# Optimization experiments

Hardware: AMD Instinct MI355X
Metric: run time of the kernel (lower is better)

Reference implementation:

```python
import jax, jax.numpy as jnp
import numpy as np

D = 192

def layer_norm(x, g, b, eps=1e-5):
    m = jnp.mean(x, -1, keepdims=True)
    v = jnp.var(x, -1, keepdims=True)
    return (x - m) * jax.lax.rsqrt(v + eps) * g + b

def _bilinear(v, x, y, H, W):
    # v: (N, nH, H*W, hd); x, y: (N, nH, Q) fractional pixel coords (grid_sample, align_corners=False, zero pad)
    x0 = jnp.floor(x); y0 = jnp.floor(y)
    wx = x - x0; wy = y - y0
    x0i = x0.astype(jnp.int32); y0i = y0.astype(jnp.int32)
    def gather(xi, yi):
        valid = (xi >= 0) & (xi < W) & (yi >= 0) & (yi < H)
        idx = jnp.clip(yi, 0, H - 1) * W + jnp.clip(xi, 0, W - 1)
        g = jnp.take_along_axis(v, idx[..., None], axis=2)
        return jnp.where(valid[..., None], g, 0.0)
    return (gather(x0i, y0i) * ((1 - wx) * (1 - wy))[..., None]
            + gather(x0i + 1, y0i) * (wx * (1 - wy))[..., None]
            + gather(x0i, y0i + 1) * ((1 - wx) * wy)[..., None]
            + gather(x0i + 1, y0i + 1) * (wx * wy)[..., None])

def _linear1d(v, p, T):
    # v: (N, nH, T, hd); p: (N, nH, Q) fractional temporal coords
    p0 = jnp.floor(p); wp = p - p0; p0i = p0.astype(jnp.int32)
    def gather(pi):
        valid = (pi >= 0) & (pi < T)
        idx = jnp.clip(pi, 0, T - 1)
        g = jnp.take_along_axis(v, idx[..., None], axis=2)
        return jnp.where(valid[..., None], g, 0.0)
    return gather(p0i) * (1 - wp)[..., None] + gather(p0i + 1) * wp[..., None]

def msdeform_2d(q, ref, H, W, nH, P, off_w, off_b, aw_w, aw_b, v_w, v_b, o_w, o_b):
    # single-level MSDeformAttn; q == input_flatten (self-attn style usage)
    N, L, d = q.shape; hd = d // nH
    v = (q @ v_w + v_b).reshape(N, L, nH, hd).transpose(0, 2, 1, 3)  # (N,nH,L,hd)
    off = (q @ off_w + off_b).reshape(N, L, nH, P, 2)
    aw = jax.nn.softmax((q @ aw_w + aw_b).reshape(N, L, nH, P), axis=-1)
    norm = jnp.array([W, H], dtype=q.dtype)
    loc = ref[:, :, None, :, :] + off / norm  # (N,L,nH,P,2)
    x = (loc[..., 0] * W - 0.5).transpose(0, 2, 1, 3).reshape(N, nH, L * P)
    y = (loc[..., 1] * H - 0.5).transpose(0, 2, 1, 3).reshape(N, nH, L * P)
    samp = _bilinear(v, x, y, H, W).reshape(N, nH, L, P, hd)
    out = jnp.einsum('nlhp,nhlpd->nlhd', aw, samp).reshape(N, L, d)
    return out @ o_w + o_b

def msdeform_1d(q, ref, T, nH, P, off_w, off_b, aw_w, aw_b, v_w, v_b, o_w, o_b):
    N, L, d = q.shape; hd = d // nH  # L == T
    v = (q @ v_w + v_b).reshape(N, L, nH, hd).transpose(0, 2, 1, 3)
    off = (q @ off_w + off_b).reshape(N, L, nH, P)
    aw = jax.nn.softmax((q @ aw_w + aw_b).reshape(N, L, nH, P), axis=-1)
    loc = ref[:, :, 0, 0][:, :, None, None] + off / T  # (N,L,nH,P)
    p = (loc * T - 0.5).transpose(0, 2, 1, 3).reshape(N, nH, L * P)
    samp = _linear1d(v, p, T).reshape(N, nH, L, P, hd)
    out = jnp.einsum('nlhp,nhlpd->nlhd', aw, samp).reshape(N, L, d)
    return out @ o_w + o_b

def setup_inputs():
    key = jax.random.key(0)
    ks = jax.random.split(key, 24)
    d = D; n, t, h, w = 2, 8, 48, 48
    f = lambda k, shape, s=0.05: jax.random.normal(k, shape, dtype=jnp.float32) * s
    return {
        'x': jax.random.normal(ks[0], (n, d, t, h, w), dtype=jnp.float32),
        'fuse': jax.random.normal(ks[1], (n, d, h, w), dtype=jnp.float32),
        'conv_w': f(ks[2], (d, 2 * d)), 'conv_b': f(ks[3], (d,)),
        's_off_w': f(ks[4], (d, 16 * 2 * 2), 0.01), 's_off_b': f(ks[5], (16 * 2 * 2,), 0.01),
        's_aw_w': f(ks[6], (d, 16 * 2)), 's_aw_b': f(ks[7], (16 * 2,)),
        's_v_w': f(ks[8], (d, d)), 's_v_b': f(ks[9], (d,)),
        's_o_w': f(ks[10], (d, d)), 's_o_b': f(ks[11], (d,)),
        't_off_w': f(ks[12], (d, 8 * 4), 0.01), 't_off_b': f(ks[13], (8 * 4,), 0.01),
        't_aw_w': f(ks[14], (d, 8 * 4)), 't_aw_b': f(ks[15], (8 * 4,)),
        't_v_w': f(ks[16], (d, d)), 't_v_b': f(ks[17], (d,)),
        't_o_w': f(ks[18], (d, d)), 't_o_b': f(ks[19], (d,)),
        'ln1_g': jnp.ones((d,), jnp.float32), 'ln1_b': jnp.zeros((d,), jnp.float32),
        'ln2_g': jnp.ones((d,), jnp.float32), 'ln2_b': jnp.zeros((d,), jnp.float32),
        'ln3_g': jnp.ones((d,), jnp.float32), 'ln3_b': jnp.zeros((d,), jnp.float32),
        'lin1_w': f(ks[20], (2 * d, d)), 'lin1_b': f(ks[21], (d,)),
        'lin2_w': f(ks[22], (d, d)), 'lin2_b': f(ks[23], (d,)),
    }

def reference(x, fuse, conv_w, conv_b, s_off_w, s_off_b, s_aw_w, s_aw_b, s_v_w, s_v_b, s_o_w, s_o_b,
              t_off_w, t_off_b, t_aw_w, t_aw_b, t_v_w, t_v_b, t_o_w, t_o_b,
              ln1_g, ln1_b, ln2_g, ln2_b, ln3_g, ln3_b, lin1_w, lin1_b, lin2_w, lin2_b):
    n, c, t, h, w = x.shape; d = c
    fuse_e = jnp.broadcast_to(fuse[:, :, None, :, :], (n, c, t, h, w))
    xc = jnp.concatenate([x, fuse_e], axis=1)                      # (n,2c,t,h,w)
    xm = jnp.einsum('ncthw,oc->nothw', xc, conv_w) + conv_b[None, :, None, None, None]
    # spatial deformable attention over h*w tokens per (n*t)
    x_space = xm.transpose(0, 2, 3, 4, 1).reshape(n * t, h * w, d)
    yy, xx = jnp.meshgrid(jnp.linspace(0, 1, h, dtype=x.dtype), jnp.linspace(0, 1, w, dtype=x.dtype), indexing='ij')
    ref2 = jnp.broadcast_to(jnp.stack([yy, xx], -1).reshape(1, h * w, 1, 2), (n * t, h * w, 1, 2))
    s_out = msdeform_2d(x_space, ref2, h, w, 16, 2, s_off_w, s_off_b, s_aw_w, s_aw_b, s_v_w, s_v_b, s_o_w, s_o_b)
    # temporal deformable attention over t tokens per (n*h*w)
    x_temp = xm.transpose(0, 3, 4, 1, 2).reshape(n * h * w, t, d)
    ref1 = jnp.broadcast_to(jnp.linspace(0, 1, t, dtype=x.dtype).reshape(1, t, 1, 1), (n * h * w, t, 1, 1))
    t_out = msdeform_1d(x_temp, ref1, t, 8, 4, t_off_w, t_off_b, t_aw_w, t_aw_b, t_v_w, t_v_b, t_o_w, t_o_b)
    # residual + LN, then the original's raw .view(h*w, t, n, c) reinterpretation (replicated faithfully)
    xs = layer_norm(x_space + s_out, ln1_g, ln1_b)
    xs = xs.reshape(h * w, t, n, d).transpose(1, 0, 2, 3).reshape(t * h * w, n, d)
    xt = layer_norm(x_temp + t_out, ln2_g, ln2_b)
    xt = xt.reshape(h * w, t, n, d).transpose(1, 0, 2, 3).reshape(t * h * w, n, d)
    x_st = jnp.concatenate([xt, xs], axis=-1)                      # (t*h*w, n, 2d)
    x_st = jax.nn.gelu(x_st @ lin1_w + lin1_b, approximate=False) @ lin2_w + lin2_b
    x_st = x_st.reshape(t, h, w, n, d).transpose(3, 4, 0, 1, 2)    # (n,d,t,h,w)
    xm = xm + x_st
    out = layer_norm(xm.transpose(0, 2, 3, 4, 1), ln3_g, ln3_b).transpose(0, 4, 1, 2, 3)
    return out
```

## Files before the change

### kernel.cpp

```cpp
#include <hip/hip_runtime.h>
#include <hip/hip_bf16.h>
#include <math.h>

typedef __hip_bfloat16 bf16;
typedef __attribute__((ext_vector_type(8))) short bf16x8;
typedef __attribute__((ext_vector_type(4))) float f32x4;

#define N_    2
#define D_    192
#define T_    8
#define H_    48
#define W_    48
#define HW_   2304
#define NPOS  36864
#define BUF_ELEMS 7077888

#define OFF_SOFFW 0
#define OFF_SOFFB 12288
#define OFF_SAWW  12352
#define OFF_SAWB  18496
#define OFF_SVW   18528
#define OFF_SVB   55392
#define OFF_SOW   55584
#define OFF_SOB   92448
#define OFF_TOFFW 92640
#define OFF_TOFFB 98784
#define OFF_TAWW  98816
#define OFF_TAWB  104960
#define OFF_TVW   104992
#define OFF_TVB   141856
#define OFF_TOW   142048
#define OFF_TOB   178912
#define OFF_LN1G  179104
#define OFF_LN1B  179296
#define OFF_LN2G  179488
#define OFF_LN2B  179680
#define OFF_LN3G  179872
#define OFF_LN3B  180064
#define OFF_LIN1W 180256
#define OFF_LIN1B 253984
#define OFF_LIN2W 254176
#define OFF_LIN2B 291040
#define OFF_CONVB 291232
#define WF_TOTAL  291424

#define PB_SCOMB 0
#define PB_SOW   55296
#define PB_TCOMB 92160
#define PB_TOW   141312
#define PB_LIN1  178176
#define PB_CONV  251904
#define PB_LIN2  325632
#define PB_TOTAL 362496

static __device__ __forceinline__ float b2f(bf16 v){ return __bfloat162float(v); }
static __device__ __forceinline__ bf16  f2b(float v){ return __float2bfloat16(v); }
static __device__ __forceinline__ float lo16(unsigned u){
  unsigned v = u<<16; return *(float*)&v;
}
static __device__ __forceinline__ float hi16(unsigned u){
  unsigned v = u & 0xFFFF0000u; return *(float*)&v;
}
static __device__ __forceinline__ unsigned pk2(float a, float b){
  bf16 x = f2b(a), y = f2b(b);
  return (unsigned)*(unsigned short*)&x | ((unsigned)*(unsigned short*)&y << 16);
}
static __device__ __forceinline__ int detect_bf(const void* ln1g){
  unsigned u = *(const unsigned*)ln1g;
  return __builtin_amdgcn_readfirstlane(((u & 0xFFFFu) != 0u) ? 1 : 0);
}
static __device__ __forceinline__ int swz8(int ch, int r){ return ch ^ (r & 7); }

struct KPtrs { const void* p[27]; };
static __device__ const int WSZ[27] = {12288,64,6144,32,36864,192,36864,192,
  6144,32,6144,32,36864,192,36864,192, 192,192,192,192,192,192, 73728,192,36864,192, 192};

__global__ void k_cvtw(KPtrs P, float* __restrict__ WF, const void* __restrict__ ln1g){
  int bf = detect_bf(ln1g);
  int gid = blockIdx.x*256 + threadIdx.x;
  if (gid >= WF_TOTAL) return;
  int e = 0, off = 0;
  while (gid >= off + WSZ[e]){ off += WSZ[e]; ++e; }
  int i = gid - off;
  WF[gid] = bf ? b2f(((const bf16*)P.p[e])[i]) : ((const float*)P.p[e])[i];
}

__global__ void k_wt(const void* __restrict__ W, float* __restrict__ Wt, const void* __restrict__ ln1g){
  int bf = detect_bf(ln1g);
  int i = blockIdx.x*256 + threadIdx.x;
  if (i < 384*192){
    int c = i/192, o = i%192;
    Wt[i] = bf ? b2f(((const bf16*)W)[o*384+c]) : ((const float*)W)[o*384+c];
  }
}

__global__ void k_packB(const float* __restrict__ WF, const float* __restrict__ Wt,
                        bf16* __restrict__ PB){
  const int NB[7]  = {108,72,96,72,144,144,72};
  const int NT[7]  = {18,12,16,12,12,12,12};
  const int DST[7] = {PB_SCOMB, PB_SOW, PB_TCOMB, PB_TOW, PB_LIN1, PB_CONV, PB_LIN2};
  int bid = blockIdx.x, e = 0, start = 0;
  while (e < 6 && bid >= start + NB[e]){ start += NB[e]; ++e; }
  int local = bid - start;
  int nt = local % NT[e], kt = local / NT[e];
  int l = threadIdx.x;
  int k0 = kt*32 + (l>>4)*8, n0 = nt*16 + (l&15);
  bf16* D = PB + DST[e] + ((long)(kt*NT[e]+nt)*64 + l)*8;
  #pragma unroll
  for (int i=0;i<8;++i){
    int k = k0 + i;
    float v;
    if (e==0){
      if (n0<192)      v = WF[OFF_SVW  + k*192 + n0];
      else if (n0<256) v = WF[OFF_SOFFW+ k*64  + (n0-192)];
      else             v = WF[OFF_SAWW + k*32  + (n0-256)];
    } else if (e==1)   v = WF[OFF_SOW  + k*192 + n0];
    else if (e==2){
      if (n0<192)      v = WF[OFF_TVW  + k*192 + n0];
      else if (n0<224) v = WF[OFF_TOFFW+ k*32  + (n0-192)];
      else             v = WF[OFF_TAWW + k*32  + (n0-224)];
    } else if (e==3)   v = WF[OFF_TOW  + k*192 + n0];
    else if (e==4)     v = WF[OFF_LIN1W+ k*192 + n0];
    else if (e==5)     v = Wt[k*192 + n0];
    else               v = WF[OFF_LIN2W+ k*192 + n0];
    D[i] = f2b(v);
  }
}

template<int KTOT, int MODE, int CF32>
__global__ void __launch_bounds__(256) k_gemm(const bf16* __restrict__ A0, const bf16* __restrict__ A1,
      const bf16* __restrict__ Bp, const float* __restrict__ bias, void* __restrict__ C_){
  __shared__ bf16 sA[64*KTOT];
  const int NCH = KTOT/8;
  int tid = threadIdx.x;
  int r0 = blockIdx.x*64;
  for (int i=tid; i<64*NCH; i+=256){
    int r = i/NCH, ch = i - r*NCH;
    int grow;
    if (MODE==1){
      int q = r0+r, f = q>>1, n2 = q&1;
      int t2 = f/HW_, hw2 = f - t2*HW_;
      grow = hw2*16 + t2*2 + n2;
    } else grow = r0+r;
    const bf16* src = (MODE==1 && ch>=24) ? (A1 + (long)grow*192 + (ch-24)*8)
                                          : (A0 + (long)grow*192 + ch*8);
    *(bf16x8*)(sA + r*KTOT + swz8(ch,r)*8) = *(const bf16x8*)src;
  }
  __syncthreads();
  int wid = tid>>6, lane = tid&63;
  int m16 = lane&15, kg = lane>>4;
  f32x4 acc[4][3];
  #pragma unroll
  for (int mi=0;mi<4;++mi)
    #pragma unroll
    for (int ni=0;ni<3;++ni) acc[mi][ni] = (f32x4){0.f,0.f,0.f,0.f};

  const int NKT = KTOT/32;
  for (int kt=0; kt<NKT; ++kt){
    bf16x8 b[3];
    #pragma unroll
    for (int ni=0;ni<3;++ni){
      int nt = wid*3 + ni;
      b[ni] = *(const bf16x8*)(Bp + ((long)(kt*12+nt)*64 + lane)*8);
    }
    bf16x8 a[4];
    #pragma unroll
    for (int mi=0;mi<4;++mi){
      int row = mi*16 + m16;
      a[mi] = *(const bf16x8*)(sA + row*KTOT + swz8(kt*4+kg,row)*8);
    }
    #pragma unroll
    for (int mi=0;mi<4;++mi)
      #pragma unroll
      for (int ni=0;ni<3;++ni)
        acc[mi][ni] = __builtin_amdgcn_mfma_f32_16x16x32_bf16(a[mi], b[ni], acc[mi][ni], 0,0,0);
  }
  const float IS2 = 0.70710678118654752f;
  #pragma unroll
  for (int mi=0;mi<4;++mi)
    #pragma unroll
    for (int ni=0;ni<3;++ni){
      int col = (wid*3+ni)*16 + m16;
      float bv = bias[col];
      #pragma unroll
      for (int rg=0;rg<4;++rg){
        int row = r0 + mi*16 + kg*4 + rg;
        float v = acc[mi][ni][rg] + bv;
        if (MODE==1) v = 0.5f*v*(1.f+erff(v*IS2));
        if (CF32) ((float*)C_)[(long)row*192 + col] = v;
        else      ((bf16*)C_)[(long)row*192 + col] = f2b(v);
      }
    }
}

template<int NWAVES, int NTW, int NO>
__global__ void __launch_bounds__(NWAVES*64) k_gemmC(const float* __restrict__ A,
      const bf16* __restrict__ Bp, const float* __restrict__ biasV,
      const float* __restrict__ biasO, const float* __restrict__ biasA,
      bf16* __restrict__ Cv, float* __restrict__ Coa){
  __shared__ bf16 sA[64*192];
  const int NT_TOT = NWAVES*NTW;
  const int NOA = NT_TOT*16 - 192;
  int tid = threadIdx.x;
  int r0 = blockIdx.x*64;
  for (int i=tid; i<64*48; i+=NWAVES*64){
    int r = i/48, c4 = i - r*48;
    float4 v = *(const float4*)(A + (long)(r0+r)*192 + c4*4);
    bf16* dst = sA + r*192 + swz8(c4>>1, r)*8 + (c4&1)*4;
    dst[0]=f2b(v.x); dst[1]=f2b(v.y); dst[2]=f2b(v.z); dst[3]=f2b(v.w);
  }
  __syncthreads();
  int wid = tid>>6, lane = tid&63;
  int m16 = lane&15, kg = lane>>4;
  f32x4 acc[4][NTW];
  #pragma unroll
  for (int mi=0;mi<4;++mi)
    #pragma unroll
    for (int ni=0;ni<NTW;++ni) acc[mi][ni] = (f32x4){0.f,0.f,0.f,0.f};
  for (int kt=0; kt<6; ++kt){
    bf16x8 b[NTW];
    #pragma unroll
    for (int ni=0;ni<NTW;++ni){
      int nt = wid*NTW + ni;
      b[ni] = *(const bf16x8*)(Bp + ((long)(kt*NT_TOT+nt)*64 + lane)*8);
    }
    bf16x8 a[4];
    #pragma unroll
    for (int mi=0;mi<4;++mi){
      int row = mi*16 + m16;
      a[mi] = *(const bf16x8*)(sA + row*192 + swz8(kt*4+kg,row)*8);
    }
    #pragma unroll
    for (int mi=0;mi<4;++mi)
      #pragma unroll
      for (int ni=0;ni<NTW;++ni)
        acc[mi][ni] = __builtin_amdgcn_mfma_f32_16x16x32_bf16(a[mi], b[ni], acc[mi][ni], 0,0,0);
  }
  #pragma unroll
  for (int mi=0;mi<4;++mi)
    #pragma unroll
    for (int ni=0;ni<NTW;++ni){
      int col = (wid*NTW+ni)*16 + m16;
      #pragma unroll
      for (int rg=0;rg<4;++rg){
        int row = r0 + mi*16 + kg*4 + rg;
        float v = acc[mi][ni][rg];
        if (col < 192)           Cv[(long)row*192 + col] = f2b(v + biasV[col]);
        else if (col < 192+NO)   Coa[(long)row*NOA + (col-192)] = v + biasO[col-192];
        else                     Coa[(long)row*NOA + (col-192)] = v + biasA[col-192-NO];
      }
    }
}

__global__ void __launch_bounds__(256) k_convm(const void* __restrict__ x, const void* __restrict__ fuse,
      const bf16* __restrict__ Bp, const float* __restrict__ bias, float* __restrict__ B0,
      const void* __restrict__ ln1g){
  __shared__ bf16 sA[64*384];
  int bf = detect_bf(ln1g);
  int bid = blockIdx.x;
  int n = bid/(8*36), rm = bid%(8*36);
  int t = rm/36, hb = rm%36;
  int hw0 = hb*64;
  int tid = threadIdx.x;
  if (bf){
    for (int i=tid; i<384*64; i+=256){
      int c = i>>6, j = i&63;
      long idx = (c<192) ? ((long)((n*192+c)*8 + t)*HW_ + hw0 + j)
                         : ((long)(n*192+(c-192))*HW_ + hw0 + j);
      bf16 v = ((const bf16*)((c<192)?x:fuse))[idx];
      sA[j*384 + swz8(c>>3, j)*8 + (c&7)] = v;
    }
  } else {
    for (int i=tid; i<384*64; i+=256){
      int c = i>>6, j = i&63;
      long idx = (c<192) ? ((long)((n*192+c)*8 + t)*HW_ + hw0 + j)
                         : ((long)(n*192+(c-192))*HW_ + hw0 + j);
      float v = ((const float*)((c<192)?x:fuse))[idx];
      sA[j*384 + swz8(c>>3, j)*8 + (c&7)] = f2b(v);
    }
  }
  __syncthreads();
  int wid = tid>>6, lane = tid&63;
  int m16 = lane&15, kg = lane>>4;
  f32x4 acc[4][3];
  #pragma unroll
  for (int mi=0;mi<4;++mi)
    #pragma unroll
    for (int ni=0;ni<3;++ni) acc[mi][ni] = (f32x4){0.f,0.f,0.f,0.f};
  for (int kt=0; kt<12; ++kt){
    bf16x8 b[3];
    #pragma unroll
    for (int ni=0;ni<3;++ni){
      int nt = wid*3 + ni;
      b[ni] = *(const bf16x8*)(Bp + ((long)(kt*12+nt)*64 + lane)*8);
    }
    bf16x8 a[4];
    #pragma unroll
    for (int mi=0;mi<4;++mi){
      int row = mi*16 + m16;
      a[mi] = *(const bf16x8*)(&sA[row*384 + swz8(kt*4+kg,row)*8]);
    }
    #pragma unroll
    for (int mi=0;mi<4;++mi)
      #pragma unroll
      for (int ni=0;ni<3;++ni)
        acc[mi][ni] = __builtin_amdgcn_mfma_f32_16x16x32_bf16(a[mi], b[ni], acc[mi][ni], 0,0,0);
  }
  long posbase = (long)(n*8+t)*HW_ + hw0;
  #pragma unroll
  for (int mi=0;mi<4;++mi)
    #pragma unroll
    for (int ni=0;ni<3;++ni){
      int col = (wid*3+ni)*16 + m16;
      float bv = bias[col];
      #pragma unroll
      for (int rg=0;rg<4;++rg){
        int row = mi*16 + kg*4 + rg;
        B0[(posbase + row)*192 + col] = acc[mi][ni][rg] + bv;
      }
    }
}

__global__ void __launch_bounds__(256) k_xt(const float* __restrict__ S0, float* __restrict__ S4){
  __shared__ float s[8*1536];
  int b0 = blockIdx.x*8, tid = threadIdx.x;
  for (int i=tid; i<8*1536; i+=256){
    int j = i/1536, rest = i - j*1536;
    int t = rest/192, o = rest - t*192;
    int b = b0 + j;
    int n = b/HW_, hw = b - n*HW_;
    s[j*1536 + (o/24)*192 + (o%24)*8 + t] = S0[((long)((n*8+t)*HW_) + hw)*192 + o];
  }
  __syncthreads();
  for (int i=tid; i<8*1536; i+=256){
    int j = i/1536, rest = i - j*1536;
    S4[(long)(b0+j)*1536 + rest] = s[j*1536 + rest];
  }
}

__global__ void __launch_bounds__(256) k_samp_s(const float* __restrict__ OA, const bf16* __restrict__ V,
    bf16* __restrict__ out){
  __shared__ float tup[512][8];
  int r0 = blockIdx.x*16, tid = threadIdx.x;
  int nt = r0 / HW_;
  {
    int row = tid>>4, head = tid&15;
    int l = (r0+row) % HW_;
    int iy = l/48, jx = l%48;
    const float* oa = OA + (long)(r0+row)*96;
    float l0 = oa[64+head*2], l1 = oa[64+head*2+1];
    float m = fmaxf(l0,l1);
    float e0 = __expf(l0-m), e1 = __expf(l1-m);
    float inv = 1.f/(e0+e1);
    const float SC = 48.0f/47.0f;
    #pragma unroll
    for (int p=0;p<2;++p){
      float aw = (p==0?e0:e1)*inv;
      float fx = iy*SC + oa[head*4+p*2+0] - 0.5f;
      float fy = jx*SC + oa[head*4+p*2+1] - 0.5f;
      float x0f = floorf(fx), y0f = floorf(fy);
      float wx = fx-x0f, wy = fy-y0f;
      int x0 = (int)x0f, y0 = (int)y0f;
      int x1 = x0+1, y1 = y0+1;
      bool vx0 = (x0>=0 && x0<48), vx1 = (x1>=0 && x1<48);
      bool vy0 = (y0>=0 && y0<48), vy1 = (y1>=0 && y1<48);
      int cx0 = min(max(x0,0),47), cx1 = min(max(x1,0),47);
      int cy0 = min(max(y0,0),47), cy1 = min(max(y1,0),47);
      float* tp = tup[row*32 + head*2 + p];
      tp[0] = (vx0&&vy0) ? aw*(1.f-wx)*(1.f-wy) : 0.f;
      tp[1] = (vx1&&vy0) ? aw*wx*(1.f-wy)       : 0.f;
      tp[2] = (vx0&&vy1) ? aw*(1.f-wx)*wy       : 0.f;
      tp[3] = (vx1&&vy1) ? aw*wx*wy             : 0.f;
      tp[4] = (float)(cy0*48+cx0);
      tp[5] = (float)(cy0*48+cx1);
      tp[6] = (float)(cy1*48+cx0);
      tp[7] = (float)(cy1*48+cx1);
    }
  }
  __syncthreads();
  const unsigned* vbu = (const unsigned*)(V + (long)nt*HW_*192);
  for (int it=tid; it<1536; it+=256){
    int row = it/96, cp = it - row*96;
    int head = cp/6;
    float a0 = 0.f, a1 = 0.f;
    #pragma unroll
    for (int p=0;p<2;++p){
      const float* tp = tup[row*32 + head*2 + p];
      #pragma unroll
      for (int c=0;c<4;++c){
        float w = tp[c];
        int idx = (int)tp[4+c];
        unsigned u = vbu[idx*96 + cp];
        a0 += w*lo16(u);
        a1 += w*hi16(u);
      }
    }
    ((unsigned*)out)[(long)(r0+row)*96 + cp] = pk2(a0, a1);
  }
}

__global__ void __launch_bounds__(256) k_samp_t(const float* __restrict__ OT, const bf16* __restrict__ V,
    bf16* __restrict__ out){
  __shared__ float tup[512][4];
  __shared__ unsigned sV[1536];
  int r0 = blockIdx.x*16, tid = threadIdx.x;
  int b0 = r0 >> 3;
  if (tid < 128){
    int row = tid>>3, head = tid&7;
    int tau = (r0+row) & 7;
    float pref = tau*(8.0f/7.0f) - 0.5f;
    const float* ot = OT + (long)(r0+row)*64;
    float l0=ot[32+head*4], l1=ot[32+head*4+1], l2=ot[32+head*4+2], l3=ot[32+head*4+3];
    float m = fmaxf(fmaxf(l0,l1), fmaxf(l2,l3));
    float e0=__expf(l0-m), e1=__expf(l1-m), e2=__expf(l2-m), e3=__expf(l3-m);
    float inv = 1.f/(e0+e1+e2+e3);
    float ee[4] = {e0,e1,e2,e3};
    #pragma unroll
    for (int p=0;p<4;++p){
      float aw = ee[p]*inv;
      float fp = pref + ot[head*4+p];
      float p0f = floorf(fp);
      float wp = fp - p0f;
      int p0 = (int)p0f, p1 = p0+1;
      float* tp = tup[row*32 + head*4 + p];
      tp[0] = (p0>=0 && p0<8) ? aw*(1.f-wp) : 0.f;
      tp[1] = (p1>=0 && p1<8) ? aw*wp       : 0.f;
      tp[2] = (float)min(max(p0,0),7);
      tp[3] = (float)min(max(p1,0),7);
    }
  } else {
    const unsigned* Vu = (const unsigned*)(V + (long)b0*1536);
    for (int i=tid-128; i<1536; i+=128) sV[i] = Vu[i];
  }
  __syncthreads();
  for (int it=tid; it<1536; it+=256){
    int row = it/96, cp = it - row*96;
    int head = cp/12;
    const unsigned* vb = sV + (row>>3)*768;
    float a0 = 0.f, a1 = 0.f;
    #pragma unroll
    for (int p=0;p<4;++p){
      const float* tp = tup[row*32 + head*4 + p];
      unsigned u0 = vb[(int)tp[2]*96 + cp];
      unsigned u1 = vb[(int)tp[3]*96 + cp];
      a0 += tp[0]*lo16(u0) + tp[1]*lo16(u1);
      a1 += tp[0]*hi16(u0) + tp[1]*hi16(u1);
    }
    ((unsigned*)out)[(long)(r0+row)*96 + cp] = pk2(a0, a1);
  }
}

__global__ void __launch_bounds__(256) k_addln(const float* __restrict__ X, const bf16* __restrict__ Y,
    const float* __restrict__ g, const float* __restrict__ bta, bf16* __restrict__ out){
  int r = blockIdx.x*4 + (threadIdx.x>>6);
  int lane = threadIdx.x & 63;
  float v[3]; float s=0.f, s2=0.f;
  #pragma unroll
  for (int e=0;e<3;++e){
    int c = lane*3+e;
    float y = X[(long)r*192+c] + b2f(Y[(long)r*192+c]);
    v[e]=y; s+=y; s2+=y*y;
  }
  #pragma unroll
  for (int off=32; off>0; off>>=1){ s += __shfl_xor(s,off); s2 += __shfl_xor(s2,off); }
  float mean = s*(1.f/192.f);
  float rstd = rsqrtf(s2*(1.f/192.f) - mean*mean + 1e-5f);
  #pragma unroll
  for (int e=0;e<3;++e){
    int c = lane*3+e;
    out[(long)r*192+c] = f2b((v[e]-mean)*rstd*g[c] + bta[c]);
  }
}

__global__ void __launch_bounds__(256) k_final3(const float* __restrict__ B0, const bf16* __restrict__ hid,
    const bf16* __restrict__ Bp, const float* __restrict__ bias2,
    const float* __restrict__ g, const float* __restrict__ bta,
    void* __restrict__ out, const void* __restrict__ ln1g){
  __shared__ float yb[32][193];
  __shared__ float mrs[32][2];
  bf16* sA = (bf16*)&yb[0][0];
  int bf = detect_bf(ln1g);
  int pos0 = blockIdx.x*32;
  int tid = threadIdx.x, wid = tid>>6, lane = tid&63;
  int m16 = lane&15, kg = lane>>4;
  int n2 = pos0/(T_*HW_), rem0 = pos0%(T_*HW_);
  long qrow0 = (long)rem0*2 + n2;
  for (int i=tid; i<32*24; i+=256){
    int r = i/24, ch = i - r*24;
    *(bf16x8*)(sA + r*192 + swz8(ch,r)*8) =
        *(const bf16x8*)(hid + (qrow0 + r*2)*192 + ch*8);
  }
  __syncthreads();
  f32x4 acc[2][3];
  #pragma unroll
  for (int mi=0;mi<2;++mi)
    #pragma unroll
    for (int ni=0;ni<3;++ni) acc[mi][ni] = (f32x4){0.f,0.f,0.f,0.f};
  for (int kt=0; kt<6; ++kt){
    bf16x8 b[3];
    #pragma unroll
    for (int ni=0;ni<3;++ni){
      int nt = wid*3 + ni;
      b[ni] = *(const bf16x8*)(Bp + ((long)(kt*12+nt)*64 + lane)*8);
    }
    bf16x8 a[2];
    #pragma unroll
    for (int mi=0;mi<2;++mi){
      int row = mi*16 + m16;
      a[mi] = *(const bf16x8*)(sA + row*192 + swz8(kt*4+kg,row)*8);
    }
    #pragma unroll
    for (int mi=0;mi<2;++mi)
      #pragma unroll
      for (int ni=0;ni<3;++ni)
        acc[mi][ni] = __builtin_amdgcn_mfma_f32_16x16x32_bf16(a[mi], b[ni], acc[mi][ni], 0,0,0);
  }
  __syncthreads();
  #pragma unroll
  for (int mi=0;mi<2;++mi)
    #pragma unroll
    for (int ni=0;ni<3;++ni){
      int col = (wid*3+ni)*16 + m16;
      float bv = bias2[col];
      #pragma unroll
      for (int rg=0;rg<4;++rg){
        int lr = mi*16 + kg*4 + rg;
        yb[lr][col] = acc[mi][ni][rg] + bv + B0[(long)(pos0+lr)*192 + col];
      }
    }
  __syncthreads();
  for (int rr=0; rr<8; ++rr){
    int row = wid*8 + rr;
    float s=0.f, s2=0.f;
    #pragma unroll
    for (int e=0;e<3;++e){
      float v = yb[row][lane*3+e];
      s += v; s2 += v*v;
    }
    #pragma unroll
    for (int off=32; off>0; off>>=1){ s += __shfl_xor(s,off); s2 += __shfl_xor(s2,off); }
    if (lane==0){
      float mean = s*(1.f/192.f);
      mrs[row][0] = mean;
      mrs[row][1] = rsqrtf(s2*(1.f/192.f) - mean*mean + 1e-5f);
    }
  }
  __syncthreads();
  int t2 = rem0/HW_, hw0 = rem0%HW_;
  int j = lane & 31;
  float mean = mrs[j][0], rstd = mrs[j][1];
  for (int cc=0; cc<48; cc+=2){
    int c = wid*48 + cc + (lane>>5);
    float val = (yb[j][c]-mean)*rstd*g[c] + bta[c];
    long idx = ((long)(n2*192 + c)*8 + t2)*HW_ + hw0 + j;
    if (bf) ((bf16*)out)[idx] = f2b(val);
    else    ((float*)out)[idx] = val;
  }
}

extern "C" void kernel_launch(void* const* d_in, const int* in_sizes, int n_in,
                              void* d_out, int out_size, void* d_ws, size_t ws_size,
                              hipStream_t stream){
  const void* x      = d_in[0];
  const void* fuse   = d_in[1];
  const void* conv_w = d_in[2];
  const void* ln1g_raw = d_in[20];

  float* S0f = (float*)d_ws;
  float* S4f = S0f + BUF_ELEMS;
  float* WS2 = S4f + BUF_ELEMS;
  bf16*  Vb  = (bf16*)WS2;
  float* OA  = WS2 + BUF_ELEMS/2;
  bf16*  HID = (bf16*)WS2;
  float* WS3 = WS2 + BUF_ELEMS;
  bf16*  ATT = (bf16*)WS3;
  float* WS4 = WS3 + BUF_ELEMS/2;
  bf16*  XS  = (bf16*)WS4;
  float* WS5 = WS4 + BUF_ELEMS/2;
  bf16*  XT  = (bf16*)WS5;
  float* WF  = WS5 + BUF_ELEMS/2;
  float* Wt  = WF + WF_TOTAL;
  bf16*  PB  = (bf16*)(Wt + 384*192);

  KPtrs P;
  for (int i=0;i<26;++i) P.p[i] = d_in[4+i];
  P.p[26] = d_in[3];

  k_cvtw <<<(WF_TOTAL+255)/256, 256, 0, stream>>>(P, WF, ln1g_raw);
  k_wt   <<<288, 256, 0, stream>>>(conv_w, Wt, ln1g_raw);
  k_packB<<<708, 64, 0, stream>>>(WF, Wt, PB);

  k_convm<<<576, 256, 0, stream>>>(x, fuse, PB+PB_CONV, WF+OFF_CONVB, S0f, ln1g_raw);
  k_xt   <<<576, 256, 0, stream>>>(S0f, S4f);

  k_gemmC<6,3,64><<<576, 384, 0, stream>>>(S0f, PB+PB_SCOMB, WF+OFF_SVB, WF+OFF_SOFFB, WF+OFF_SAWB, Vb, OA);
  k_samp_s<<<NPOS/16, 256, 0, stream>>>(OA, Vb, ATT);
  k_gemm<192,0,0><<<576, 256, 0, stream>>>(ATT, nullptr, PB+PB_SOW, WF+OFF_SOB, ATT);
  k_addln<<<NPOS/4, 256, 0, stream>>>(S0f, ATT, WF+OFF_LN1G, WF+OFF_LN1B, XS);

  k_gemmC<4,4,32><<<576, 256, 0, stream>>>(S4f, PB+PB_TCOMB, WF+OFF_TVB, WF+OFF_TOFFB, WF+OFF_TAWB, Vb, OA);
  k_samp_t<<<NPOS/16, 256, 0, stream>>>(OA, Vb, ATT);
  k_gemm<192,0,0><<<576, 256, 0, stream>>>(ATT, nullptr, PB+PB_TOW, WF+OFF_TOB, ATT);
  k_addln<<<NPOS/4, 256, 0, stream>>>(S4f, ATT, WF+OFF_LN2G, WF+OFF_LN2B, XT);

  k_gemm<384,1,0><<<576, 256, 0, stream>>>(XT, XS, PB+PB_LIN1, WF+OFF_LIN1B, HID);
  k_final3<<<NPOS/32, 256, 0, stream>>>(S0f, HID, PB+PB_LIN2, WF+OFF_LIN2B,
                                        WF+OFF_LN3G, WF+OFF_LN3B, d_out, ln1g_raw);
}
```

Measured before the change: 218.9 us.

## Fuse deformable sampling, output projection, residual and LayerNorm into one kernel

Replaces the three-kernel sequence of sampling, output-projection GEMM and add+LayerNorm with a single kernel each for the spatial and temporal branches. Sampled rows are written straight into swizzled shared memory, multiplied with MFMA against the packed projection weights, then combined with bias and residual and normalized in shared memory. This removes the bf16 ATT round trip through global memory and two launches per branch. In exchange each block uses more shared memory and does more serialized phases, which may lower occupancy, and the small 32-row GEMM tile reloads B weights from global in every block.

Result: no change. 218.9 us (-0.0%).

```diff
diff --git a/kernel.cpp b/kernel.cpp
--- a/kernel.cpp
+++ b/kernel.cpp
@@ -338,13 +338,19 @@
   }
 }
 
-__global__ void __launch_bounds__(256) k_samp_s(const float* __restrict__ OA, const bf16* __restrict__ V,
-    bf16* __restrict__ out){
-  __shared__ float tup[512][8];
-  int r0 = blockIdx.x*16, tid = threadIdx.x;
+__global__ void __launch_bounds__(256) k_sfuse(const float* __restrict__ OA, const bf16* __restrict__ V,
+    const bf16* __restrict__ Bp, const float* __restrict__ biasO,
+    const float* __restrict__ X, const float* __restrict__ g, const float* __restrict__ bta,
+    bf16* __restrict__ outXS){
+  __shared__ char smem[32768 + 12288];
+  __shared__ float mrs[32][2];
+  float (*tup)[8] = (float(*)[8])smem;
+  float (*yb)[193] = (float(*)[193])smem;
+  bf16* sA = (bf16*)(smem + 32768);
+  int r0 = blockIdx.x*32, tid = threadIdx.x;
   int nt = r0 / HW_;
-  {
-    int row = tid>>4, head = tid&15;
+  for (int i=tid; i<512; i+=256){
+    int row = i>>4, head = i&15;
     int l = (r0+row) % HW_;
     int iy = l/48, jx = l%48;
     const float* oa = OA + (long)(r0+row)*96;
@@ -379,7 +385,7 @@
   }
   __syncthreads();
   const unsigned* vbu = (const unsigned*)(V + (long)nt*HW_*192);
-  for (int it=tid; it<1536; it+=256){
+  for (int it=tid; it<3072; it+=256){
     int row = it/96, cp = it - row*96;
     int head = cp/6;
     float a0 = 0.f, a1 = 0.f;
@@ -395,17 +401,89 @@
         a1 += w*hi16(u);
       }
     }
-    ((unsigned*)out)[(long)(r0+row)*96 + cp] = pk2(a0, a1);
-  }
-}
-
-__global__ void __launch_bounds__(256) k_samp_t(const float* __restrict__ OT, const bf16* __restrict__ V,
-    bf16* __restrict__ out){
-  __shared__ float tup[512][4];
-  __shared__ unsigned sV[1536];
-  int r0 = blockIdx.x*16, tid = threadIdx.x;
+    *(unsigned*)(sA + row*192 + swz8(cp>>2,row)*8 + (cp&3)*2) = pk2(a0,a1);
+  }
+  __syncthreads();
+  int wid = tid>>6, lane = tid&63;
+  int m16 = lane&15, kg = lane>>4;
+  f32x4 acc[2][3];
+  #pragma unroll
+  for (int mi=0;mi<2;++mi)
+    #pragma unroll
+    for (int ni=0;ni<3;++ni) acc[mi][ni] = (f32x4){0.f,0.f,0.f,0.f};
+  for (int kt=0; kt<6; ++kt){
+    bf16x8 b[3];
+    #pragma unroll
+    for (int ni=0;ni<3;++ni){
+      int ntb = wid*3 + ni;
+      b[ni] = *(const bf16x8*)(Bp + ((long)(kt*12+ntb)*64 + lane)*8);
+    }
+    bf16x8 a[2];
+    #pragma unroll
+    for (int mi=0;mi<2;++mi){
+      int row = mi*16 + m16;
+      a[mi] = *(const bf16x8*)(sA + row*192 + swz8(kt*4+kg,row)*8);
+    }
+    #pragma unroll
+    for (int mi=0;mi<2;++mi)
+      #pragma unroll
+      for (int ni=0;ni<3;++ni)
+        acc[mi][ni] = __builtin_amdgcn_mfma_f32_16x16x32_bf16(a[mi], b[ni], acc[mi][ni], 0,0,0);
+  }
+  __syncthreads();
+  #pragma unroll
+  for (int mi=0;mi<2;++mi)
+    #pragma unroll
+    for (int ni=0;ni<3;++ni){
+      int col = (wid*3+ni)*16 + m16;
+      float bv = biasO[col];
+      #pragma unroll
+      for (int rg=0;rg<4;++rg){
+        int lr = mi*16 + kg*4 + rg;
+        yb[lr][col] = acc[mi][ni][rg] + bv + X[(long)(r0+lr)*192 + col];
+      }
+    }
+  __syncthreads();
+  for (int rr=0; rr<8; ++rr){
+    int row = wid*8 + rr;
+    float s=0.f, s2=0.f;
+    #pragma unroll
+    for (int e=0;e<3;++e){
+      float v = yb[row][lane*3+e];
+      s += v; s2 += v*v;
+    }
+    #pragma unroll
+    for (int off=32; off>0; off>>=1){ s += __shfl_xor(s,off); s2 += __shfl_xor(s2,off); }
+    if (lane==0){
+      float mean = s*(1.f/192.f);
+      mrs[row][0] = mean;
+      mrs[row][1] = rsqrtf(s2*(1.f/192.f) - mean*mean + 1e-5f);
+    }
+  }
+  __syncthreads();
+  for (int i=tid; i<3072; i+=256){
+    int row = i/96, cp = i - row*96;
+    float mean = mrs[row][0], rstd = mrs[row][1];
+    int c0 = cp*2, c1 = c0+1;
+    float v0 = (yb[row][c0]-mean)*rstd*g[c0] + bta[c0];
+    float v1 = (yb[row][c1]-mean)*rstd*g[c1] + bta[c1];
+    ((unsigned*)outXS)[(long)(r0+row)*96 + cp] = pk2(v0,v1);
+  }
+}
+
+__global__ void __launch_bounds__(256) k_tfuse(const float* __restrict__ OT, const bf16* __restrict__ V,
+    const bf16* __restrict__ Bp, const float* __restrict__ biasO,
+    const float* __restrict__ X, const float* __restrict__ g, const float* __restrict__ bta,
+    bf16* __restrict__ outXT){
+  __shared__ char smem[24704 + 12288];
+  __shared__ unsigned sV[3072];
+  __shared__ float mrs[32][2];
+  float (*tup)[4] = (float(*)[4])smem;
+  float (*yb)[193] = (float(*)[193])smem;
+  bf16* sA = (bf16*)(smem + 24704);
+  int r0 = blockIdx.x*32, tid = threadIdx.x;
   int b0 = r0 >> 3;
-  if (tid < 128){
+  {
     int row = tid>>3, head = tid&7;
     int tau = (r0+row) & 7;
     float pref = tau*(8.0f/7.0f) - 0.5f;
@@ -428,12 +506,13 @@
       tp[2] = (float)min(max(p0,0),7);
       tp[3] = (float)min(max(p1,0),7);
     }
-  } else {
+  }
+  {
     const unsigned* Vu = (const unsigned*)(V + (long)b0*1536);
-    for (int i=tid-128; i<1536; i+=128) sV[i] = Vu[i];
-  }
-  __syncthreads();
-  for (int it=tid; it<1536; it+=256){
+    for (int i=tid; i<3072; i+=256) sV[i] = Vu[i];
+  }
+  __syncthreads();
+  for (int it=tid; it<3072; it+=256){
     int row = it/96, cp = it - row*96;
     int head = cp/12;
     const unsigned* vb = sV + (row>>3)*768;
@@ -446,29 +525,73 @@
       a0 += tp[0]*lo16(u0) + tp[1]*lo16(u1);
       a1 += tp[0]*hi16(u0) + tp[1]*hi16(u1);
     }
-    ((unsigned*)out)[(long)(r0+row)*96 + cp] = pk2(a0, a1);
-  }
-}
-
-__global__ void __launch_bounds__(256) k_addln(const float* __restrict__ X, const bf16* __restrict__ Y,
-    const float* __restrict__ g, const float* __restrict__ bta, bf16* __restrict__ out){
-  int r = blockIdx.x*4 + (threadIdx.x>>6);
-  int lane = threadIdx.x & 63;
-  float v[3]; float s=0.f, s2=0.f;
-  #pragma unroll
-  for (int e=0;e<3;++e){
-    int c = lane*3+e;
-    float y = X[(long)r*192+c] + b2f(Y[(long)r*192+c]);
-    v[e]=y; s+=y; s2+=y*y;
-  }
-  #pragma unroll
-  for (int off=32; off>0; off>>=1){ s += __shfl_xor(s,off); s2 += __shfl_xor(s2,off); }
-  float mean = s*(1.f/192.f);
-  float rstd = rsqrtf(s2*(1.f/192.f) - mean*mean + 1e-5f);
-  #pragma unroll
-  for (int e=0;e<3;++e){
-    int c = lane*3+e;
-    out[(long)r*192+c] = f2b((v[e]-mean)*rstd*g[c] + bta[c]);
+    *(unsigned*)(sA + row*192 + swz8(cp>>2,row)*8 + (cp&3)*2) = pk2(a0,a1);
+  }
+  __syncthreads();
+  int wid = tid>>6, lane = tid&63;
+  int m16 = lane&15, kg = lane>>4;
+  f32x4 acc[2][3];
+  #pragma unroll
+  for (int mi=0;mi<2;++mi)
+    #pragma unroll
+    for (int ni=0;ni<3;++ni) acc[mi][ni] = (f32x4){0.f,0.f,0.f,0.f};
+  for (int kt=0; kt<6; ++kt){
+    bf16x8 b[3];
+    #pragma unroll
+    for (int ni=0;ni<3;++ni){
+      int ntb = wid*3 + ni;
+      b[ni] = *(const bf16x8*)(Bp + ((long)(kt*12+ntb)*64 + lane)*8);
+    }
+    bf16x8 a[2];
+    #pragma unroll
+    for (int mi=0;mi<2;++mi){
+      int row = mi*16 + m16;
+      a[mi] = *(const bf16x8*)(sA + row*192 + swz8(kt*4+kg,row)*8);
+    }
+    #pragma unroll
+    for (int mi=0;mi<2;++mi)
+      #pragma unroll
+      for (int ni=0;ni<3;++ni)
+        acc[mi][ni] = __builtin_amdgcn_mfma_f32_16x16x32_bf16(a[mi], b[ni], acc[mi][ni], 0,0,0);
+  }
+  __syncthreads();
+  #pragma unroll
+  for (int mi=0;mi<2;++mi)
+    #pragma unroll
+    for (int ni=0;ni<3;++ni){
+      int col = (wid*3+ni)*16 + m16;
+      float bv = biasO[col];
+      #pragma unroll
+      for (int rg=0;rg<4;++rg){
+        int lr = mi*16 + kg*4 + rg;
+        yb[lr][col] = acc[mi][ni][rg] + bv + X[(long)(r0+lr)*192 + col];
+      }
+    }
+  __syncthreads();
+  for (int rr=0; rr<8; ++rr){
+    int row = wid*8 + rr;
+    float s=0.f, s2=0.f;
+    #pragma unroll
+    for (int e=0;e<3;++e){
+      float v = yb[row][lane*3+e];
+      s += v; s2 += v*v;
+    }
+    #pragma unroll
+    for (int off=32; off>0; off>>=1){ s += __shfl_xor(s,off); s2 += __shfl_xor(s2,off); }
+    if (lane==0){
+      float mean = s*(1.f/192.f);
+      mrs[row][0] = mean;
+      mrs[row][1] = rsqrtf(s2*(1.f/192.f) - mean*mean + 1e-5f);
+    }
+  }
+  __syncthreads();
+  for (int i=tid; i<3072; i+=256){
+    int row = i/96, cp = i - row*96;
+    float mean = mrs[row][0], rstd = mrs[row][1];
+    int c0 = cp*2, c1 = c0+1;
+    float v0 = (yb[row][c0]-mean)*rstd*g[c0] + bta[c0];
+    float v1 = (yb[row][c1]-mean)*rstd*g[c1] + bta[c1];
+    ((unsigned*)outXT)[(long)(r0+row)*96 + cp] = pk2(v0,v1);
   }
 }
 
@@ -572,9 +695,7 @@
   bf16*  Vb  = (bf16*)WS2;
   float* OA  = WS2 + BUF_ELEMS/2;
   bf16*  HID = (bf16*)WS2;
-  float* WS3 = WS2 + BUF_ELEMS;
-  bf16*  ATT = (bf16*)WS3;
-  float* WS4 = WS3 + BUF_ELEMS/2;
+  float* WS4 = WS2 + BUF_ELEMS;
   bf16*  XS  = (bf16*)WS4;
   float* WS5 = WS4 + BUF_ELEMS/2;
   bf16*  XT  = (bf16*)WS5;
@@ -594,14 +715,12 @@
   k_xt   <<<576, 256, 0, stream>>>(S0f, S4f);
 
   k_gemmC<6,3,64><<<576, 384, 0, stream>>>(S0f, PB+PB_SCOMB, WF+OFF_SVB, WF+OFF_SOFFB, WF+OFF_SAWB, Vb, OA);
-  k_samp_s<<<NPOS/16, 256, 0, stream>>>(OA, Vb, ATT);
-  k_gemm<192,0,0><<<576, 256, 0, stream>>>(ATT, nullptr, PB+PB_SOW, WF+OFF_SOB, ATT);
-  k_addln<<<NPOS/4, 256, 0, stream>>>(S0f, ATT, WF+OFF_LN1G, WF+OFF_LN1B, XS);
+  k_sfuse<<<NPOS/32, 256, 0, stream>>>(OA, Vb, PB+PB_SOW, WF+OFF_SOB, S0f,
+                                       WF+OFF_LN1G, WF+OFF_LN1B, XS);
 
   k_gemmC<4,4,32><<<576, 256, 0, stream>>>(S4f, PB+PB_TCOMB, WF+OFF_TVB, WF+OFF_TOFFB, WF+OFF_TAWB, Vb, OA);
-  k_samp_t<<<NPOS/16, 256, 0, stream>>>(OA, Vb, ATT);
-  k_gemm<192,0,0><<<576, 256, 0, stream>>>(ATT, nullptr, PB+PB_TOW, WF+OFF_TOB, ATT);
-  k_addln<<<NPOS/4, 256, 0, stream>>>(S4f, ATT, WF+OFF_LN2G, WF+OFF_LN2B, XT);
+  k_tfuse<<<NPOS/32, 256, 0, stream>>>(OA, Vb, PB+PB_TOW, WF+OFF_TOB, S4f,
+                                       WF+OFF_LN2G, WF+OFF_LN2B, XT);
 
   k_gemm<384,1,0><<<576, 256, 0, stream>>>(XT, XS, PB+PB_LIN1, WF+OFF_LIN1B, HID);
   k_final3<<<NPOS/32, 256, 0, stream>>>(S0f, HID, PB+PB_LIN2, WF+OFF_LIN2B,
```
